# Performance work log

Hardware: AMD Instinct MI355X
Metric: run time of the kernel (lower is better)

The kernel has to match this reference:

```python
import jax, jax.numpy as jnp
import numpy as np

SEQ = 128; HID = 2048; NH = 8; NKV = 2; NREP = NH // NKV; HD = 256; FF = 4096
PLD = 256; NLT = 35; NLAYERS = 8; WIN = 512; FULL_LEN = 2048; PAST = 1024
FULL_LAYERS = {5}  # Gemma3 pattern: full attention when (i+1) % 6 == 0
PLE_PROJ_SCALE = HID ** -0.5
PLE_IN_SCALE = 0.7071067811865476  # rsqrt(2)
NEG = -1e9


def _rms(x, w, eps=1e-6):
    return x * jax.lax.rsqrt(jnp.mean(x * x, -1, keepdims=True) + eps) * w


def _vnorm(x, eps=1e-6):
    return x * jax.lax.rsqrt(jnp.mean(x * x, -1, keepdims=True) + eps)


def _rope(x, cos, sin):
    # x: (1, H, S, hd); cos/sin: (1, S, hd)
    c = cos[:, None]; s = sin[:, None]
    h = x.shape[-1] // 2
    x1, x2 = x[..., :h], x[..., h:]
    return x * c + jnp.concatenate([-x2, x1], -1) * s


def _rope_tables(pos, theta):
    inv = 1.0 / (theta ** (np.arange(0, HD, 2, dtype=np.float32) / HD))
    ang = pos[:, None] * inv[None, :]
    emb = np.concatenate([ang, ang], -1)  # (S, HD)
    return jnp.asarray(np.cos(emb), jnp.float32)[None], jnp.asarray(np.sin(emb), jnp.float32)[None]


def setup_inputs() -> dict:
    key = jax.random.key(0)
    ks = iter(jax.random.split(key, 64))
    f = lambda shape, s=0.02: jax.random.normal(next(ks), shape, dtype=jnp.float32) * s
    inp = {}
    inp['hidden_states'] = f((1, SEQ, HID), 1.0)
    inp['per_layer_raw'] = f((1, SEQ, NLT * PLD), 1.0)
    pos = np.arange(PAST, PAST + SEQ, dtype=np.float32)
    inp['cos_s'], inp['sin_s'] = _rope_tables(pos, 10000.0)
    inp['cos_f'], inp['sin_f'] = _rope_tables(pos, 1000000.0)
    i_s = np.arange(SEQ); j_f = np.arange(FULL_LEN); j_s = np.arange(WIN)
    inp['causal_mask_full'] = jnp.asarray(np.where(j_f[None, :] <= PAST + i_s[:, None], 0.0, NEG).astype(np.float32))[None, None]
    inp['causal_mask_sliding'] = jnp.asarray(np.where(j_s[None, :] <= WIN - SEQ + i_s[:, None], 0.0, NEG).astype(np.float32))[None, None]
    ind = np.zeros((FULL_LEN, SEQ), np.float32); ind[PAST + i_s, i_s] = 1.0
    inp['update_indicator'] = jnp.asarray(ind)[None, None]
    inp['K_sliding'] = f((7, NKV, WIN, HD), 1.0); inp['V_sliding'] = f((7, NKV, WIN, HD), 1.0)
    inp['K_full'] = f((1, NKV, FULL_LEN, HD), 1.0); inp['V_full'] = f((1, NKV, FULL_LEN, HD), 1.0)
    # learned parameters (stacked over the 8 layers)
    inp['Wq'] = f((NLAYERS, HID, NH * HD)); inp['Wk'] = f((NLAYERS, HID, NKV * HD))
    inp['Wv'] = f((NLAYERS, HID, NKV * HD)); inp['Wo'] = f((NLAYERS, NH * HD, HID))
    inp['w_in_ln'] = jnp.ones((NLAYERS, HID)); inp['w_q_norm'] = jnp.ones((NLAYERS, HD))
    inp['w_k_norm'] = jnp.ones((NLAYERS, HD)); inp['w_post_attn_ln'] = jnp.ones((NLAYERS, HID))
    inp['w_pre_ff_ln'] = jnp.ones((NLAYERS, HID))
    inp['Wgate'] = f((NLAYERS, HID, FF)); inp['Wup'] = f((NLAYERS, HID, FF)); inp['Wdown'] = f((NLAYERS, FF, HID))
    inp['w_post_ff_ln'] = jnp.ones((NLAYERS, HID))
    inp['Wple_gate'] = f((NLAYERS, HID, PLD)); inp['Wple_proj'] = f((NLAYERS, PLD, HID))
    inp['w_post_ple_ln'] = jnp.ones((NLAYERS, HID))
    inp['layer_scalar'] = jnp.ones((NLAYERS,))
    inp['Wple_model_proj'] = f((HID, NLT * PLD)); inp['w_ple_norm'] = jnp.ones((PLD,))
    return inp


def _forward(hidden_states, per_layer_raw, cos_s, sin_s, cos_f, sin_f,
             causal_mask_full, causal_mask_sliding, update_indicator,
             K_sliding, V_sliding, K_full, V_full,
             Wq, Wk, Wv, Wo, w_in_ln, w_q_norm, w_k_norm, w_post_attn_ln,
             w_pre_ff_ln, Wgate, Wup, Wdown, w_post_ff_ln,
             Wple_gate, Wple_proj, w_post_ple_ln, layer_scalar,
             Wple_model_proj, w_ple_norm):
    S = hidden_states.shape[1]
    # PLE: project hidden, per-layer RMSNorm over pld groups, combine with raw per-layer inputs
    proj = (hidden_states @ Wple_model_proj) * PLE_PROJ_SCALE  # (1,S,NLT*PLD)
    proj = _rms(proj.reshape(S, NLT, PLD), w_ple_norm)
    raw = per_layer_raw.reshape(S, NLT, PLD)
    ple = ((proj + raw) * PLE_IN_SCALE).reshape(1, S, NLT * PLD)

    hs = hidden_states
    Ks, Vs, Kf, Vf = K_sliding, V_sliding, K_full, V_full
    new_ks, new_vs = [], []
    si = 0; fi = 0
    for i in range(NLAYERS):
        is_full = i in FULL_LAYERS
        cos, sin = (cos_f, sin_f) if is_full else (cos_s, sin_s)
        res = hs
        h = _rms(hs, w_in_ln[i])
        # Q/K norm is per (token, head) RMS over head_dim, then RoPE
        q = _rms((h @ Wq[i]).reshape(1, S, NH, HD), w_q_norm[i]).transpose(0, 2, 1, 3)
        q = _rope(q, cos, sin)
        k = _rms((h @ Wk[i]).reshape(1, S, NKV, HD), w_k_norm[i]).transpose(0, 2, 1, 3)
        k = _rope(k, cos, sin)
        v = _vnorm((h @ Wv[i]).reshape(1, S, NKV, HD).transpose(0, 2, 1, 3))
        new_ks.append(k); new_vs.append(v)
        if is_full:
            # matmul-based indicator scatter into the full-attention cache slot
            k_sc = jnp.matmul(update_indicator, k)  # (1,NKV,FULL_LEN,HD)
            v_sc = jnp.matmul(update_indicator, v)
            cm = jnp.sum(update_indicator, -1, keepdims=True)  # (1,1,FULL_LEN,1)
            Kf = Kf.at[fi:fi + 1].set(Kf[fi:fi + 1] * (1.0 - cm) + k_sc)
            Vf = Vf.at[fi:fi + 1].set(Vf[fi:fi + 1] * (1.0 - cm) + v_sc)
            K_attn, V_attn, mask = Kf[fi:fi + 1], Vf[fi:fi + 1], causal_mask_full
            fi += 1
        else:
            # sliding-window shift: drop oldest S, append new K/V
            nk = jnp.concatenate([Ks[si:si + 1, :, S:, :], k], axis=2)
            nv = jnp.concatenate([Vs[si:si + 1, :, S:, :], v], axis=2)
            Ks = Ks.at[si:si + 1].set(nk); Vs = Vs.at[si:si + 1].set(nv)
            K_attn, V_attn, mask = nk, nv, causal_mask_sliding
            si += 1
        Ke = jnp.repeat(K_attn, NREP, axis=1)  # GQA repeat_interleave
        Ve = jnp.repeat(V_attn, NREP, axis=1)
        aw = jax.nn.softmax(jnp.einsum('bhsd,bhld->bhsl', q, Ke) + mask, axis=-1)  # no 1/sqrt(hd), as in source
        attn = jnp.einsum('bhsl,bhld->bhsd', aw, Ve).transpose(0, 2, 1, 3).reshape(1, S, NH * HD)
        hs = res + _rms(attn @ Wo[i], w_post_attn_ln[i])
        res = hs
        h2 = _rms(hs, w_pre_ff_ln[i])
        mlp = (jax.nn.gelu(h2 @ Wgate[i], approximate=True) * (h2 @ Wup[i])) @ Wdown[i]
        hs = res + _rms(mlp, w_post_ff_ln[i])
        res = hs
        pls = ple[:, :, i * PLD:(i + 1) * PLD]
        g = jax.nn.gelu(hs @ Wple_gate[i], approximate=True) * pls
        hs = res + _rms(g @ Wple_proj[i], w_post_ple_ln[i])
        hs = hs * layer_scalar[i]
    return hs, jnp.stack(new_ks), jnp.stack(new_vs)


def reference(hidden_states, per_layer_raw, cos_s, sin_s, cos_f, sin_f,
              causal_mask_full, causal_mask_sliding, update_indicator,
              K_sliding, V_sliding, K_full, V_full,
              Wq, Wk, Wv, Wo, w_in_ln, w_q_norm, w_k_norm, w_post_attn_ln,
              w_pre_ff_ln, Wgate, Wup, Wdown, w_post_ff_ln,
              Wple_gate, Wple_proj, w_post_ple_ln, layer_scalar,
              Wple_model_proj, w_ple_norm):
    return _forward(hidden_states, per_layer_raw, cos_s, sin_s, cos_f, sin_f,
                    causal_mask_full, causal_mask_sliding, update_indicator,
                    K_sliding, V_sliding, K_full, V_full,
                    Wq, Wk, Wv, Wo, w_in_ln, w_q_norm, w_k_norm, w_post_attn_ln,
                    w_pre_ff_ln, Wgate, Wup, Wdown, w_post_ff_ln,
                    Wple_gate, Wple_proj, w_post_ple_ln, layer_scalar,
                    Wple_model_proj, w_ple_norm)
```

## Files before the change

kernel.cpp:

```cpp
#include <hip/hip_runtime.h>
#include <stdint.h>

typedef short s16x8 __attribute__((ext_vector_type(8)));
typedef float f32x4 __attribute__((ext_vector_type(4)));
typedef unsigned short u16;

#define MFMA16(a,b,c) __builtin_amdgcn_mfma_f32_16x16x32_bf16((a),(b),(c),0,0,0)
#define ACAP 1184

__device__ __forceinline__ u16 f2bf(float f) {
  union { float f; unsigned u; } v; v.f = f;
  return (u16)((v.u + 0x7FFFu + ((v.u >> 16) & 1u)) >> 16);
}
__device__ __forceinline__ float bf2f(u16 u) {
  union { float f; unsigned v; } x; x.v = ((unsigned)u) << 16; return x.f;
}

__device__ __forceinline__ float block_sum256(float v, float* lred) {
  #pragma unroll
  for (int d = 32; d >= 1; d >>= 1) v += __shfl_xor(v, d);
  __syncthreads();
  if ((threadIdx.x & 63) == 0) lred[threadIdx.x >> 6] = v;
  __syncthreads();
  return (lred[0] + lred[1]) + (lred[2] + lred[3]);
}

__device__ __forceinline__ float gelu_t(float x) {
  float u = 0.7978845608028654f * (x + 0.044715f * x * x * x);
  return 0.5f * x * (1.0f + tanhf(u));
}

__global__ __launch_bounds__(256) void gemm3_k(
    const u16* __restrict__ Ah, const u16* __restrict__ Al, int lda,
    const float* __restrict__ W0, const float* __restrict__ W1, const float* __restrict__ W2,
    int e0, int e1, int ld0, int ld1, int ld2,
    float* __restrict__ out, int N, int kchunk, int Ktot)
{
  __shared__ float red[4 * 2048];
  const int n0 = blockIdx.x * 16;
  const int split = blockIdx.y;
  const float* W; int ldw, c0;
  if (n0 < e0)      { W = W0; ldw = ld0; c0 = n0; }
  else if (n0 < e1) { W = W1; ldw = ld1; c0 = n0 - e0; }
  else              { W = W2; ldw = ld2; c0 = n0 - e1; }
  const int w = threadIdx.x >> 6, l = threadIdx.x & 63;
  const int lr = l & 15, lh = l >> 4;
  const int wk = kchunk >> 2;
  const int k0 = split * kchunk + w * wk, k1 = k0 + wk;
  const u16* Abh = Ah + (size_t)lr * lda + 8 * lh;
  const u16* Abl = Al + (size_t)lr * lda + 8 * lh;
  const float* Wb = W + (size_t)(8 * lh) * ldw + (c0 + lr);

  f32x4 acc[8];
  #pragma unroll
  for (int i = 0; i < 8; i++) acc[i] = (f32x4){0.f,0.f,0.f,0.f};

  for (int k = k0; k < k1; k += 32) {
    s16x8 ah[8], al[8];
    #pragma unroll
    for (int mt = 0; mt < 8; mt++) {
      ah[mt] = *(const s16x8*)(Abh + (size_t)(16*mt)*lda + k);
      al[mt] = *(const s16x8*)(Abl + (size_t)(16*mt)*lda + k);
    }
    s16x8 bh, bl;
    #pragma unroll
    for (int jj = 0; jj < 8; jj++) {
      float wv = Wb[(size_t)(k + jj) * ldw];
      u16 hb = f2bf(wv);
      bh[jj] = (short)hb;
      bl[jj] = (short)f2bf(wv - bf2f(hb));
    }
    #pragma unroll
    for (int mt = 0; mt < 8; mt++) acc[mt] = MFMA16(ah[mt], bh, acc[mt]);
    #pragma unroll
    for (int mt = 0; mt < 8; mt++) acc[mt] = MFMA16(ah[mt], bl, acc[mt]);
    #pragma unroll
    for (int mt = 0; mt < 8; mt++) acc[mt] = MFMA16(al[mt], bh, acc[mt]);
  }
  #pragma unroll
  for (int mt = 0; mt < 8; mt++)
    #pragma unroll
    for (int r = 0; r < 4; r++)
      red[w * 2048 + (16*mt + 4*lh + r) * 16 + lr] = acc[mt][r];
  __syncthreads();
  const size_t ob = (size_t)split * (128 * (size_t)N) + n0;
  #pragma unroll
  for (int i = 0; i < 8; i++) {
    int e = threadIdx.x + 256 * i;
    int row = e >> 4, c = e & 15;
    float s = (red[e] + red[2048 + e]) + (red[4096 + e] + red[6144 + e]);
    out[ob + (size_t)row * N + c] = s;
  }
}

__global__ __launch_bounds__(256) void init_k(
    const float* __restrict__ hid, const float* __restrict__ w0,
    float* __restrict__ hs, u16* __restrict__ h0b, u16* __restrict__ h0l,
    u16* __restrict__ hbf, u16* __restrict__ hbl)
{
  __shared__ float lred[4];
  int s = blockIdx.x, t = threadIdx.x;
  float x[8]; float ss = 0.f;
  #pragma unroll
  for (int i = 0; i < 8; i++) {
    int j = t + 256 * i;
    float v = hid[(size_t)s * 2048 + j];
    x[i] = v; ss += v * v;
    hs[(size_t)s * 2048 + j] = v;
    u16 hi = f2bf(v);
    h0b[(size_t)s * 2048 + j] = hi;
    h0l[(size_t)s * 2048 + j] = f2bf(v - bf2f(hi));
  }
  ss = block_sum256(ss, lred);
  float rs = rsqrtf(ss * (1.f/2048.f) + 1e-6f);
  #pragma unroll
  for (int i = 0; i < 8; i++) {
    int j = t + 256 * i;
    float xn = x[i] * rs * w0[j];
    u16 hi = f2bf(xn);
    hbf[(size_t)s * 2048 + j] = hi;
    hbl[(size_t)s * 2048 + j] = f2bf(xn - bf2f(hi));
  }
}

__global__ __launch_bounds__(256) void ple_norm_k(
    const float* __restrict__ proj, const float* __restrict__ raw,
    const float* __restrict__ wp, float* __restrict__ ple)
{
  __shared__ float lred[4];
  int b = blockIdx.x;
  int s = b / 35, lt = b % 35, t = threadIdx.x;
  size_t idx = (size_t)s * 8960 + lt * 256 + t;
  float p = proj[idx] * 0.022097086912079612f;
  float ss = block_sum256(p * p, lred);
  float rs = rsqrtf(ss * (1.f/256.f) + 1e-6f);
  ple[idx] = (p * rs * wp[t] + raw[idx]) * 0.7071067811865476f;
}

__global__ __launch_bounds__(256) void fill_kv2_k(
    const float* __restrict__ oK, const float* __restrict__ oV,
    u16* __restrict__ Kh, u16* __restrict__ Kl,
    u16* __restrict__ VTh, u16* __restrict__ VTl,
    int olen, int ooff, int old_ld, int nA)
{
  __shared__ float tile[64][65];
  int b = blockIdx.x, t = threadIdx.x;
  if (b < nA) {
    size_t base = (size_t)b * 4096;
    #pragma unroll
    for (int i = 0; i < 16; i++) {
      size_t e = base + t + 256 * i;
      int kv = (int)(e / ((size_t)olen * 256));
      size_t rem = e - (size_t)kv * olen * 256;
      int j = (int)(rem >> 8), d = (int)(rem & 255);
      float v = oK[((size_t)kv * old_ld + ooff + j) * 256 + d];
      u16 hi = f2bf(v);
      size_t dst = (size_t)kv * (ACAP*256) + (size_t)j * 256 + d;
      Kh[dst] = hi;
      Kl[dst] = f2bf(v - bf2f(hi));
    }
  } else {
    int tb = b - nA;
    int tj = olen >> 6;
    int per_kv = tj * 4;
    int kv = tb / per_kv, rem = tb % per_kv;
    int j0 = (rem % tj) * 64, d0 = (rem / tj) * 64;
    #pragma unroll
    for (int i = 0; i < 16; i++) {
      int e = t + 256 * i;
      int jj = e >> 6, dd = e & 63;
      tile[jj][dd] = oV[((size_t)kv * old_ld + ooff + j0 + jj) * 256 + d0 + dd];
    }
    __syncthreads();
    #pragma unroll
    for (int i = 0; i < 16; i++) {
      int e = t + 256 * i;
      int dd = e >> 6, jj = e & 63;
      float v = tile[jj][dd];
      u16 hi = f2bf(v);
      size_t dst = (size_t)kv * (256*ACAP) + (size_t)(d0 + dd) * ACAP + (j0 + jj);
      VTh[dst] = hi;
      VTl[dst] = f2bf(v - bf2f(hi));
    }
  }
}

__global__ __launch_bounds__(256) void prep_attn_k(
    const float* __restrict__ qkvP, int nsplit,
    const float* __restrict__ wq, const float* __restrict__ wk,
    const float* __restrict__ cosb, const float* __restrict__ sinb,
    u16* __restrict__ qh, u16* __restrict__ ql,
    float* __restrict__ outk, float* __restrict__ outv,
    u16* __restrict__ Kh, u16* __restrict__ Kl,
    u16* __restrict__ VTh, u16* __restrict__ VTl, int jbase)
{
  __shared__ float lred[4];
  __shared__ float xs[256];
  int s = blockIdx.x, t = threadIdx.x;
  const float* base = qkvP + (size_t)s * 3072;
  float c = cosb[s * 256 + t], sn = sinb[s * 256 + t];
  #pragma unroll 1
  for (int h = 0; h < 8; h++) {
    float v = 0.f;
    for (int sp = 0; sp < nsplit; sp++) v += base[(size_t)sp * (128*3072) + h * 256 + t];
    float ss = block_sum256(v * v, lred);
    float rs = rsqrtf(ss * (1.f/256.f) + 1e-6f);
    float xn = v * rs * wq[t];
    xs[t] = xn;
    __syncthreads();
    float pr = xs[t ^ 128];
    float ro = (t < 128) ? -pr : pr;
    float qv = xn * c + ro * sn;
    u16 hi = f2bf(qv);
    qh[((size_t)h * 128 + s) * 256 + t] = hi;
    ql[((size_t)h * 128 + s) * 256 + t] = f2bf(qv - bf2f(hi));
    __syncthreads();
  }
  #pragma unroll 1
  for (int g = 0; g < 2; g++) {
    float v = 0.f;
    for (int sp = 0; sp < nsplit; sp++) v += base[(size_t)sp * (128*3072) + 2048 + g * 256 + t];
    float ss = block_sum256(v * v, lred);
    float rs = rsqrtf(ss * (1.f/256.f) + 1e-6f);
    float xn = v * rs * wk[t];
    xs[t] = xn;
    __syncthreads();
    float pr = xs[t ^ 128];
    float ro = (t < 128) ? -pr : pr;
    float kq = xn * c + ro * sn;
    outk[(size_t)g * (128*256) + s * 256 + t] = kq;
    u16 khi = f2bf(kq);
    size_t kdst = (size_t)g * (ACAP*256) + (size_t)(jbase + s) * 256 + t;
    Kh[kdst] = khi;
    Kl[kdst] = f2bf(kq - bf2f(khi));
    __syncthreads();
    float vv = 0.f;
    for (int sp = 0; sp < nsplit; sp++) vv += base[(size_t)sp * (128*3072) + 2560 + g * 256 + t];
    float ss2 = block_sum256(vv * vv, lred);
    float rs2 = rsqrtf(ss2 * (1.f/256.f) + 1e-6f);
    float vn = vv * rs2;
    outv[(size_t)g * (128*256) + s * 256 + t] = vn;
    u16 vhi = f2bf(vn);
    size_t vdst = (size_t)g * (256*ACAP) + (size_t)t * ACAP + (jbase + s);
    VTh[vdst] = vhi;
    VTl[vdst] = f2bf(vn - bf2f(vhi));
  }
}

__global__ __launch_bounds__(256, 1) void attn5_k(
    const u16* __restrict__ qh, const u16* __restrict__ ql,
    const u16* __restrict__ Kh, const u16* __restrict__ Kl,
    const u16* __restrict__ VTh, const u16* __restrict__ VTl,
    u16* __restrict__ outbf, u16* __restrict__ outlo, int off)
{
  __shared__ float OW[3][16][256];
  __shared__ float MW[4][16];
  __shared__ float LW[4][16];
  __shared__ u16 Ph[4][16*32];
  __shared__ u16 Pl[4][16*32];
  int bx = blockIdx.x;
  int h = bx >> 3, qt = bx & 7;
  int kv = h >> 2;
  int s0 = qt * 16;
  int nkeys = off + s0 + 16;
  int w = threadIdx.x >> 6, l = threadIdx.x & 63;
  int lr = l & 15, lh = l >> 4;
  int ck = ((nkeys + 127) >> 7) << 5;
  int jb = w * ck;
  int je = min(jb + ck, nkeys);
  const u16* Khb = Kh + (size_t)kv * (ACAP * 256);
  const u16* Klb = Kl + (size_t)kv * (ACAP * 256);
  const u16* Vhb = VTh + (size_t)kv * (256 * (size_t)ACAP);
  const u16* Vlb = VTl + (size_t)kv * (256 * (size_t)ACAP);

  s16x8 aqh[8], aql[8];
  {
    const u16* qrh = qh + ((size_t)h * 128 + s0 + lr) * 256 + 8 * lh;
    const u16* qrl = ql + ((size_t)h * 128 + s0 + lr) * 256 + 8 * lh;
    #pragma unroll
    for (int kk = 0; kk < 8; kk++) {
      aqh[kk] = *(const s16x8*)(qrh + kk * 32);
      aql[kk] = *(const s16x8*)(qrl + kk * 32);
    }
  }
  f32x4 accO[16];
  #pragma unroll
  for (int i = 0; i < 16; i++) accO[i] = (f32x4){0.f,0.f,0.f,0.f};
  float m_run[4], l_run[4];
  #pragma unroll
  for (int r = 0; r < 4; r++) { m_run[r] = -3.0e38f; l_run[r] = 0.f; }
  u16* Pwh = &Ph[w][0];
  u16* Pwl = &Pl[w][0];

  for (int j0 = jb; j0 < je; j0 += 32) {
    f32x4 lg[2];
    lg[0] = (f32x4){0.f,0.f,0.f,0.f};
    lg[1] = (f32x4){0.f,0.f,0.f,0.f};
    #pragma unroll
    for (int kk = 0; kk < 8; kk++) {
      const u16* kb0 = Khb + (size_t)(j0 + lr) * 256 + kk * 32 + 8 * lh;
      const u16* kb1 = Khb + (size_t)(j0 + 16 + lr) * 256 + kk * 32 + 8 * lh;
      const u16* kl0 = Klb + (size_t)(j0 + lr) * 256 + kk * 32 + 8 * lh;
      const u16* kl1 = Klb + (size_t)(j0 + 16 + lr) * 256 + kk * 32 + 8 * lh;
      s16x8 b0h = *(const s16x8*)kb0, b1h = *(const s16x8*)kb1;
      s16x8 b0l = *(const s16x8*)kl0, b1l = *(const s16x8*)kl1;
      lg[0] = MFMA16(aqh[kk], b0h, lg[0]);
      lg[1] = MFMA16(aqh[kk], b1h, lg[1]);
      lg[0] = MFMA16(aqh[kk], b0l, lg[0]);
      lg[1] = MFMA16(aqh[kk], b1l, lg[1]);
      lg[0] = MFMA16(aql[kk], b0h, lg[0]);
      lg[1] = MFMA16(aql[kk], b1h, lg[1]);
    }
    float tmax[4];
    #pragma unroll
    for (int r = 0; r < 4; r++) tmax[r] = -1.0e30f;
    #pragma unroll
    for (int tt = 0; tt < 2; tt++) {
      int j = j0 + 16 * tt + lr;
      #pragma unroll
      for (int r = 0; r < 4; r++)
        if (j <= off + s0 + 4 * lh + r) tmax[r] = fmaxf(tmax[r], lg[tt][r]);
    }
    #pragma unroll
    for (int d = 1; d < 16; d <<= 1)
      #pragma unroll
      for (int r = 0; r < 4; r++) tmax[r] = fmaxf(tmax[r], __shfl_xor(tmax[r], d));
    float scl[4], rsum[4];
    #pragma unroll
    for (int r = 0; r < 4; r++) {
      float mn = fmaxf(m_run[r], tmax[r]);
      scl[r] = __expf(m_run[r] - mn);
      m_run[r] = mn;
      rsum[r] = 0.f;
    }
    #pragma unroll
    for (int tt = 0; tt < 2; tt++) {
      int j = j0 + 16 * tt + lr;
      #pragma unroll
      for (int r = 0; r < 4; r++) {
        bool valid = (j <= off + s0 + 4 * lh + r);
        float p = valid ? __expf(lg[tt][r] - m_run[r]) : 0.f;
        lg[tt][r] = p;
        rsum[r] += p;
      }
    }
    #pragma unroll
    for (int d = 1; d < 16; d <<= 1)
      #pragma unroll
      for (int r = 0; r < 4; r++) rsum[r] += __shfl_xor(rsum[r], d);
    #pragma unroll
    for (int r = 0; r < 4; r++) l_run[r] = l_run[r] * scl[r] + rsum[r];
    #pragma unroll
    for (int tt = 0; tt < 2; tt++) {
      #pragma unroll
      for (int r = 0; r < 4; r++) {
        float p = lg[tt][r];
        u16 phi = f2bf(p);
        Pwh[(4 * lh + r) * 32 + 16 * tt + lr] = phi;
        Pwl[(4 * lh + r) * 32 + 16 * tt + lr] = f2bf(p - bf2f(phi));
      }
    }
    #pragma unroll
    for (int t2 = 0; t2 < 16; t2++)
      #pragma unroll
      for (int r = 0; r < 4; r++) accO[t2][r] *= scl[r];
    s16x8 pah = *(const s16x8*)(Pwh + lr * 32 + 8 * lh);
    s16x8 pal = *(const s16x8*)(Pwl + lr * 32 + 8 * lh);
    #pragma unroll
    for (int t2 = 0; t2 < 16; t2++) {
      s16x8 bvh = *(const s16x8*)(Vhb + (size_t)(16 * t2 + lr) * ACAP + j0 + 8 * lh);
      s16x8 bvl = *(const s16x8*)(Vlb + (size_t)(16 * t2 + lr) * ACAP + j0 + 8 * lh);
      accO[t2] = MFMA16(pah, bvh, accO[t2]);
      accO[t2] = MFMA16(pah, bvl, accO[t2]);
      accO[t2] = MFMA16(pal, bvh, accO[t2]);
    }
  }
  if (w > 0) {
    #pragma unroll
    for (int t2 = 0; t2 < 16; t2++)
      #pragma unroll
      for (int r = 0; r < 4; r++)
        OW[w - 1][4 * lh + r][16 * t2 + lr] = accO[t2][r];
  }
  if (lr == 0) {
    #pragma unroll
    for (int r = 0; r < 4; r++) { MW[w][4 * lh + r] = m_run[r]; LW[w][4 * lh + r] = l_run[r]; }
  }
  __syncthreads();
  if (w == 0) {
    float ew[4][4], inv[4];
    #pragma unroll
    for (int r = 0; r < 4; r++) {
      int row = 4 * lh + r;
      float M = fmaxf(fmaxf(m_run[r], MW[1][row]), fmaxf(MW[2][row], MW[3][row]));
      ew[r][0] = __expf(m_run[r] - M);
      ew[r][1] = __expf(MW[1][row] - M);
      ew[r][2] = __expf(MW[2][row] - M);
      ew[r][3] = __expf(MW[3][row] - M);
      float L = l_run[r] * ew[r][0] + LW[1][row] * ew[r][1] + LW[2][row] * ew[r][2] + LW[3][row] * ew[r][3];
      inv[r] = 1.f / L;
    }
    #pragma unroll
    for (int t2 = 0; t2 < 16; t2++) {
      #pragma unroll
      for (int r = 0; r < 4; r++) {
        int row = 4 * lh + r, c = 16 * t2 + lr;
        float o = accO[t2][r] * ew[r][0] + OW[0][row][c] * ew[r][1]
                + OW[1][row][c] * ew[r][2] + OW[2][row][c] * ew[r][3];
        float val = o * inv[r];
        u16 hi = f2bf(val);
        outbf[(size_t)(s0 + row) * 2048 + h * 256 + c] = hi;
        outlo[(size_t)(s0 + row) * 2048 + h * 256 + c] = f2bf(val - bf2f(hi));
      }
    }
  }
}

__global__ __launch_bounds__(256) void norm_res_k(
    const float* __restrict__ parts, int nsplit,
    const float* __restrict__ wn, float* __restrict__ hs,
    const float* __restrict__ w2, u16* __restrict__ outbf, u16* __restrict__ outlo,
    const float* __restrict__ scp, float* __restrict__ outf)
{
  __shared__ float lred[4];
  int row = blockIdx.x, t = threadIdx.x;
  const float* pr = parts + (size_t)row * 2048;
  float x[8]; float ss = 0.f;
  #pragma unroll
  for (int i = 0; i < 8; i++) {
    int j = t + 256 * i;
    float v = 0.f;
    for (int sp = 0; sp < nsplit; sp++) v += pr[(size_t)sp * (128*2048) + j];
    x[i] = v; ss += v * v;
  }
  ss = block_sum256(ss, lred);
  float rs = rsqrtf(ss * (1.f/2048.f) + 1e-6f);
  float sc = scp ? scp[0] : 1.f;
  float y[8]; float ss2 = 0.f;
  #pragma unroll
  for (int i = 0; i < 8; i++) {
    int j = t + 256 * i;
    float v = (hs[(size_t)row * 2048 + j] + x[i] * rs * wn[j]) * sc;
    y[i] = v; ss2 += v * v;
    hs[(size_t)row * 2048 + j] = v;
    if (outf) outf[(size_t)row * 2048 + j] = v;
  }
  if (outbf) {
    if (w2) {
      ss2 = block_sum256(ss2, lred);
      float rs2 = rsqrtf(ss2 * (1.f/2048.f) + 1e-6f);
      #pragma unroll
      for (int i = 0; i < 8; i++) {
        int j = t + 256 * i;
        float xn = y[i] * rs2 * w2[j];
        u16 hi = f2bf(xn);
        outbf[(size_t)row * 2048 + j] = hi;
        if (outlo) outlo[(size_t)row * 2048 + j] = f2bf(xn - bf2f(hi));
      }
    } else {
      #pragma unroll
      for (int i = 0; i < 8; i++) {
        int j = t + 256 * i;
        u16 hi = f2bf(y[i]);
        outbf[(size_t)row * 2048 + j] = hi;
        if (outlo) outlo[(size_t)row * 2048 + j] = f2bf(y[i] - bf2f(hi));
      }
    }
  }
}

__global__ __launch_bounds__(256) void mlp_act_k(
    const float* __restrict__ gu, int nsplit, u16* __restrict__ out, u16* __restrict__ outlo)
{
  int base = blockIdx.x * 1024 + threadIdx.x * 4;
  int row = base >> 12, j = base & 4095;
  float g[4] = {0,0,0,0}, u[4] = {0,0,0,0};
  for (int sp = 0; sp < nsplit; sp++) {
    const float4 gg = *(const float4*)(gu + (size_t)sp * (128*8192) + (size_t)row * 8192 + j);
    const float4 uu = *(const float4*)(gu + (size_t)sp * (128*8192) + (size_t)row * 8192 + 4096 + j);
    g[0]+=gg.x; g[1]+=gg.y; g[2]+=gg.z; g[3]+=gg.w;
    u[0]+=uu.x; u[1]+=uu.y; u[2]+=uu.z; u[3]+=uu.w;
  }
  size_t ob = (size_t)row * 4096 + j;
  #pragma unroll
  for (int q = 0; q < 4; q++) {
    float val = gelu_t(g[q]) * u[q];
    u16 hi = f2bf(val);
    out[ob + q] = hi;
    outlo[ob + q] = f2bf(val - bf2f(hi));
  }
}

__global__ __launch_bounds__(256) void ple_act_k(
    const float* __restrict__ pgP, int nsplit, const float* __restrict__ ple,
    int layer, u16* __restrict__ gbf, u16* __restrict__ gbl)
{
  int s = blockIdx.x, t = threadIdx.x;
  float x = 0.f;
  for (int sp = 0; sp < nsplit; sp++) x += pgP[(size_t)sp * (128*256) + s * 256 + t];
  float val = gelu_t(x) * ple[(size_t)s * 8960 + layer * 256 + t];
  u16 hi = f2bf(val);
  gbf[s * 256 + t] = hi;
  gbl[s * 256 + t] = f2bf(val - bf2f(hi));
}

extern "C" void kernel_launch(void* const* d_in, const int* in_sizes, int n_in,
                              void* d_out, int out_size, void* d_ws, size_t ws_size,
                              hipStream_t stream)
{
  const float* hid   = (const float*)d_in[0];
  const float* raw   = (const float*)d_in[1];
  const float* cos_s = (const float*)d_in[2];
  const float* sin_s = (const float*)d_in[3];
  const float* cos_f = (const float*)d_in[4];
  const float* sin_f = (const float*)d_in[5];
  const float* Ksl   = (const float*)d_in[9];
  const float* Vsl   = (const float*)d_in[10];
  const float* Kfu   = (const float*)d_in[11];
  const float* Vfu   = (const float*)d_in[12];
  const float* Wq    = (const float*)d_in[13];
  const float* Wk    = (const float*)d_in[14];
  const float* Wv    = (const float*)d_in[15];
  const float* Wo    = (const float*)d_in[16];
  const float* w_in  = (const float*)d_in[17];
  const float* w_qn  = (const float*)d_in[18];
  const float* w_kn  = (const float*)d_in[19];
  const float* w_pa  = (const float*)d_in[20];
  const float* w_pf  = (const float*)d_in[21];
  const float* Wg    = (const float*)d_in[22];
  const float* Wu    = (const float*)d_in[23];
  const float* Wd    = (const float*)d_in[24];
  const float* w_ff  = (const float*)d_in[25];
  const float* Wpg   = (const float*)d_in[26];
  const float* Wpp   = (const float*)d_in[27];
  const float* w_pp  = (const float*)d_in[28];
  const float* lsc   = (const float*)d_in[29];
  const float* Wpm   = (const float*)d_in[30];
  const float* w_pn  = (const float*)d_in[31];

  char* ws = (char*)d_ws;
  size_t off = 0;
  auto alloc = [&](size_t b) { size_t o = off; off += (b + 255) & ~(size_t)255; return o; };
  size_t o_hs   = alloc(128*2048*4);
  size_t o_qkvP = alloc(2ull*128*3072*4);
  size_t o_t1P  = alloc(2ull*128*2048*4);
  size_t o_guP  = alloc(1ull*128*8192*4);
  size_t o_t2P  = alloc(2ull*128*2048*4);
  size_t o_pgP  = alloc(4ull*128*256*4);
  size_t o_t3P  = alloc(1ull*128*2048*4);
  size_t o_ple  = alloc(128ull*8960*4);
  size_t o_h0b  = alloc(128*2048*2);
  size_t o_h0l  = alloc(128*2048*2);
  size_t o_hb   = alloc(128*2048*2);
  size_t o_hbl  = alloc(128*2048*2);
  size_t o_h2b  = alloc(128*2048*2);
  size_t o_h2l  = alloc(128*2048*2);
  size_t o_hrb  = alloc(128*2048*2);
  size_t o_hrl  = alloc(128*2048*2);
  size_t o_ab   = alloc(128*2048*2);
  size_t o_abl  = alloc(128*2048*2);
  size_t o_mb   = alloc(128ull*4096*2);
  size_t o_mbl  = alloc(128ull*4096*2);
  size_t o_gb   = alloc(128*256*2);
  size_t o_gbl  = alloc(128*256*2);
  size_t o_qh   = alloc(8ull*128*256*2);
  size_t o_ql   = alloc(8ull*128*256*2);
  size_t o_Kh   = alloc(2ull*ACAP*256*2);
  size_t o_Kl   = alloc(2ull*ACAP*256*2);
  size_t o_VTh  = alloc(2ull*256*ACAP*2);
  size_t o_VTl  = alloc(2ull*256*ACAP*2);

  float* hs   = (float*)(ws + o_hs);
  float* qkvP = (float*)(ws + o_qkvP);
  float* t1P  = (float*)(ws + o_t1P);
  float* guP  = (float*)(ws + o_guP);
  float* t2P  = (float*)(ws + o_t2P);
  float* pgP  = (float*)(ws + o_pgP);
  float* t3P  = (float*)(ws + o_t3P);
  float* ple  = (float*)(ws + o_ple);
  float* proj = (float*)(ws + o_qkvP);
  u16* h0b = (u16*)(ws + o_h0b);
  u16* h0l = (u16*)(ws + o_h0l);
  u16* hb  = (u16*)(ws + o_hb);
  u16* hbl = (u16*)(ws + o_hbl);
  u16* h2b = (u16*)(ws + o_h2b);
  u16* h2l = (u16*)(ws + o_h2l);
  u16* hrb = (u16*)(ws + o_hrb);
  u16* hrl = (u16*)(ws + o_hrl);
  u16* ab  = (u16*)(ws + o_ab);
  u16* abl = (u16*)(ws + o_abl);
  u16* mb  = (u16*)(ws + o_mb);
  u16* mbl = (u16*)(ws + o_mbl);
  u16* gb  = (u16*)(ws + o_gb);
  u16* gbl = (u16*)(ws + o_gbl);
  u16* qhb = (u16*)(ws + o_qh);
  u16* qlb = (u16*)(ws + o_ql);
  u16* Khc = (u16*)(ws + o_Kh);
  u16* Klc = (u16*)(ws + o_Kl);
  u16* VThc = (u16*)(ws + o_VTh);
  u16* VTlc = (u16*)(ws + o_VTl);

  float* ouths = (float*)d_out;
  float* outk  = ouths + 128*2048;
  float* outv  = outk + 8*2*128*256;

  init_k<<<128, 256, 0, stream>>>(hid, w_in, hs, h0b, h0l, hb, hbl);
  gemm3_k<<<dim3(560,1), 256, 0, stream>>>(h0b, h0l, 2048, Wpm, Wpm, Wpm,
      8960, 8960, 8960, 8960, 8960, proj, 8960, 2048, 2048);
  ple_norm_k<<<128*35, 256, 0, stream>>>(proj, raw, w_pn, ple);

  for (int i = 0; i < 8; i++) {
    bool full = (i == 5);
    int si = (i < 5) ? i : i - 1;
    const float* cs = full ? cos_f : cos_s;
    const float* sn = full ? sin_f : sin_s;
    int jbase = full ? 1024 : 384;
    if (full) {
      fill_kv2_k<<<256, 256, 0, stream>>>(Kfu, Vfu, Khc, Klc, VThc, VTlc, 1024, 0, 2048, 128);
    } else {
      fill_kv2_k<<<96, 256, 0, stream>>>(Ksl + (size_t)si*2*512*256, Vsl + (size_t)si*2*512*256,
                                         Khc, Klc, VThc, VTlc, 384, 128, 512, 48);
    }
    gemm3_k<<<dim3(192,2), 256, 0, stream>>>(hb, hbl, 2048,
        Wq + (size_t)i*2048*2048, Wk + (size_t)i*2048*512, Wv + (size_t)i*2048*512,
        2048, 2560, 2048, 512, 512, qkvP, 3072, 1024, 2048);
    prep_attn_k<<<128, 256, 0, stream>>>(qkvP, 2, w_qn + i*256, w_kn + i*256, cs, sn,
        qhb, qlb, outk + (size_t)i*65536, outv + (size_t)i*65536, Khc, Klc, VThc, VTlc, jbase);
    attn5_k<<<64, 256, 0, stream>>>(qhb, qlb, Khc, Klc, VThc, VTlc, ab, abl, jbase);
    gemm3_k<<<dim3(128,2), 256, 0, stream>>>(ab, abl, 2048,
        Wo + (size_t)i*2048*2048, Wo, Wo, 2048, 2048, 2048, 2048, 2048,
        t1P, 2048, 1024, 2048);
    norm_res_k<<<128, 256, 0, stream>>>(t1P, 2, w_pa + i*2048, hs,
        w_pf + i*2048, h2b, h2l, nullptr, nullptr);
    gemm3_k<<<dim3(512,1), 256, 0, stream>>>(h2b, h2l, 2048,
        Wg + (size_t)i*2048*4096, Wu + (size_t)i*2048*4096, Wu,
        4096, 8192, 4096, 4096, 4096, guP, 8192, 2048, 2048);
    mlp_act_k<<<512, 256, 0, stream>>>(guP, 1, mb, mbl);
    gemm3_k<<<dim3(128,2), 256, 0, stream>>>(mb, mbl, 4096,
        Wd + (size_t)i*4096*2048, Wd, Wd, 2048, 2048, 2048, 2048, 2048,
        t2P, 2048, 2048, 4096);
    norm_res_k<<<128, 256, 0, stream>>>(t2P, 2, w_ff + i*2048, hs,
        nullptr, hrb, hrl, nullptr, nullptr);
    gemm3_k<<<dim3(16,4), 256, 0, stream>>>(hrb, hrl, 2048,
        Wpg + (size_t)i*2048*256, Wpg, Wpg, 256, 256, 256, 256, 256,
        pgP, 256, 512, 2048);
    ple_act_k<<<128, 256, 0, stream>>>(pgP, 4, ple, i, gb, gbl);
    gemm3_k<<<dim3(128,1), 256, 0, stream>>>(gb, gbl, 256,
        Wpp + (size_t)i*256*2048, Wpp, Wpp, 2048, 2048, 2048, 2048, 2048,
        t3P, 2048, 256, 256);
    norm_res_k<<<128, 256, 0, stream>>>(t3P, 1, w_pp + i*2048, hs,
        (i < 7) ? (w_in + (i+1)*2048) : nullptr,
        (i < 7) ? hb : nullptr,
        (i < 7) ? hbl : nullptr,
        lsc + i, (i == 7) ? ouths : nullptr);
  }
}
```

Measured before the change: 2.604 ms.

## Split attention keys across four blocks with combine kernel; prefetch GEMM weights

Attention now launches 256 blocks instead of 64, each covering a quarter of the key range. Partial unnormalized outputs plus max and sum statistics go to a workspace, and a new combine kernel merges them into the bf16 hi/lo output. This targets low occupancy, since 64 blocks on a many-CU GPU leave most units idle, at the cost of an extra launch and fp32 partial traffic. Separately, the split-bf16 GEMM now software-prefetches the next K-step's weight values into registers to hide global load latency.

```diff
diff --git a/kernel.cpp b/kernel.cpp
--- a/kernel.cpp
+++ b/kernel.cpp
@@ -55,6 +55,10 @@
   #pragma unroll
   for (int i = 0; i < 8; i++) acc[i] = (f32x4){0.f,0.f,0.f,0.f};
 
+  float bc[8];
+  #pragma unroll
+  for (int jj = 0; jj < 8; jj++) bc[jj] = Wb[(size_t)(k0 + jj) * ldw];
+
   for (int k = k0; k < k1; k += 32) {
     s16x8 ah[8], al[8];
     #pragma unroll
@@ -62,13 +66,17 @@
       ah[mt] = *(const s16x8*)(Abh + (size_t)(16*mt)*lda + k);
       al[mt] = *(const s16x8*)(Abl + (size_t)(16*mt)*lda + k);
     }
+    float bn[8];
+    if (k + 32 < k1) {
+      #pragma unroll
+      for (int jj = 0; jj < 8; jj++) bn[jj] = Wb[(size_t)(k + 32 + jj) * ldw];
+    }
     s16x8 bh, bl;
     #pragma unroll
     for (int jj = 0; jj < 8; jj++) {
-      float wv = Wb[(size_t)(k + jj) * ldw];
-      u16 hb = f2bf(wv);
+      u16 hb = f2bf(bc[jj]);
       bh[jj] = (short)hb;
-      bl[jj] = (short)f2bf(wv - bf2f(hb));
+      bl[jj] = (short)f2bf(bc[jj] - bf2f(hb));
     }
     #pragma unroll
     for (int mt = 0; mt < 8; mt++) acc[mt] = MFMA16(ah[mt], bh, acc[mt]);
@@ -76,6 +84,10 @@
     for (int mt = 0; mt < 8; mt++) acc[mt] = MFMA16(ah[mt], bl, acc[mt]);
     #pragma unroll
     for (int mt = 0; mt < 8; mt++) acc[mt] = MFMA16(al[mt], bh, acc[mt]);
+    if (k + 32 < k1) {
+      #pragma unroll
+      for (int jj = 0; jj < 8; jj++) bc[jj] = bn[jj];
+    }
   }
   #pragma unroll
   for (int mt = 0; mt < 8; mt++)
@@ -247,11 +259,11 @@
   }
 }
 
-__global__ __launch_bounds__(256, 1) void attn5_k(
+__global__ __launch_bounds__(256) void attn6_k(
     const u16* __restrict__ qh, const u16* __restrict__ ql,
     const u16* __restrict__ Kh, const u16* __restrict__ Kl,
     const u16* __restrict__ VTh, const u16* __restrict__ VTl,
-    u16* __restrict__ outbf, u16* __restrict__ outlo, int off)
+    float* __restrict__ Opart, float* __restrict__ ML, int off)
 {
   __shared__ float OW[3][16][256];
   __shared__ float MW[4][16];
@@ -259,15 +271,18 @@
   __shared__ u16 Ph[4][16*32];
   __shared__ u16 Pl[4][16*32];
   int bx = blockIdx.x;
-  int h = bx >> 3, qt = bx & 7;
+  int ks = bx & 3;
+  int b64 = bx >> 2;
+  int h = b64 >> 3, qt = b64 & 7;
   int kv = h >> 2;
   int s0 = qt * 16;
   int nkeys = off + s0 + 16;
   int w = threadIdx.x >> 6, l = threadIdx.x & 63;
   int lr = l & 15, lh = l >> 4;
-  int ck = ((nkeys + 127) >> 7) << 5;
-  int jb = w * ck;
-  int je = min(jb + ck, nkeys);
+  int cw = ((nkeys + 511) >> 9) << 5;
+  int g = ks * 4 + w;
+  int jb = g * cw;
+  int je = min(jb + cw, nkeys);
   const u16* Khb = Kh + (size_t)kv * (ACAP * 256);
   const u16* Klb = Kl + (size_t)kv * (ACAP * 256);
   const u16* Vhb = VTh + (size_t)kv * (256 * (size_t)ACAP);
@@ -388,7 +403,8 @@
   }
   __syncthreads();
   if (w == 0) {
-    float ew[4][4], inv[4];
+    float ew[4][4];
+    float Mrow[4], Lrow[4];
     #pragma unroll
     for (int r = 0; r < 4; r++) {
       int row = 4 * lh + r;
@@ -397,9 +413,10 @@
       ew[r][1] = __expf(MW[1][row] - M);
       ew[r][2] = __expf(MW[2][row] - M);
       ew[r][3] = __expf(MW[3][row] - M);
-      float L = l_run[r] * ew[r][0] + LW[1][row] * ew[r][1] + LW[2][row] * ew[r][2] + LW[3][row] * ew[r][3];
-      inv[r] = 1.f / L;
-    }
+      Lrow[r] = l_run[r] * ew[r][0] + LW[1][row] * ew[r][1] + LW[2][row] * ew[r][2] + LW[3][row] * ew[r][3];
+      Mrow[r] = M;
+    }
+    float* Ob = Opart + (size_t)bx * 4096;
     #pragma unroll
     for (int t2 = 0; t2 < 16; t2++) {
       #pragma unroll
@@ -407,12 +424,47 @@
         int row = 4 * lh + r, c = 16 * t2 + lr;
         float o = accO[t2][r] * ew[r][0] + OW[0][row][c] * ew[r][1]
                 + OW[1][row][c] * ew[r][2] + OW[2][row][c] * ew[r][3];
-        float val = o * inv[r];
-        u16 hi = f2bf(val);
-        outbf[(size_t)(s0 + row) * 2048 + h * 256 + c] = hi;
-        outlo[(size_t)(s0 + row) * 2048 + h * 256 + c] = f2bf(val - bf2f(hi));
+        Ob[row * 256 + c] = o;
       }
     }
+    if (lr == 0) {
+      #pragma unroll
+      for (int r = 0; r < 4; r++) {
+        int row = 4 * lh + r;
+        ML[bx * 32 + row] = Mrow[r];
+        ML[bx * 32 + 16 + row] = Lrow[r];
+      }
+    }
+  }
+}
+
+__global__ __launch_bounds__(256) void attn_comb_k(
+    const float* __restrict__ Opart, const float* __restrict__ ML,
+    u16* __restrict__ outbf, u16* __restrict__ outlo)
+{
+  int b = blockIdx.x;
+  int h = b >> 3, qt = b & 7, s0 = qt * 16;
+  int c = threadIdx.x;
+  #pragma unroll 1
+  for (int row = 0; row < 16; row++) {
+    float m[4], lv[4];
+    #pragma unroll
+    for (int ks = 0; ks < 4; ks++) {
+      m[ks]  = ML[(b * 4 + ks) * 32 + row];
+      lv[ks] = ML[(b * 4 + ks) * 32 + 16 + row];
+    }
+    float Mg = fmaxf(fmaxf(m[0], m[1]), fmaxf(m[2], m[3]));
+    float L = 0.f, o = 0.f;
+    #pragma unroll
+    for (int ks = 0; ks < 4; ks++) {
+      float e = __expf(m[ks] - Mg);
+      L += lv[ks] * e;
+      o += Opart[((size_t)(b * 4 + ks)) * 4096 + row * 256 + c] * e;
+    }
+    float val = o / L;
+    u16 hi = f2bf(val);
+    outbf[(size_t)(s0 + row) * 2048 + h * 256 + c] = hi;
+    outlo[(size_t)(s0 + row) * 2048 + h * 256 + c] = f2bf(val - bf2f(hi));
   }
 }
 
@@ -569,6 +621,8 @@
   size_t o_Kl   = alloc(2ull*ACAP*256*2);
   size_t o_VTh  = alloc(2ull*256*ACAP*2);
   size_t o_VTl  = alloc(2ull*256*ACAP*2);
+  size_t o_Op   = alloc(256ull*4096*4);
+  size_t o_ML   = alloc(256ull*32*4);
 
   float* hs   = (float*)(ws + o_hs);
   float* qkvP = (float*)(ws + o_qkvP);
@@ -599,6 +653,8 @@
   u16* Klc = (u16*)(ws + o_Kl);
   u16* VThc = (u16*)(ws + o_VTh);
   u16* VTlc = (u16*)(ws + o_VTl);
+  float* Opart = (float*)(ws + o_Op);
+  float* MLb   = (float*)(ws + o_ML);
 
   float* ouths = (float*)d_out;
   float* outk  = ouths + 128*2048;
@@ -626,7 +682,8 @@
         2048, 2560, 2048, 512, 512, qkvP, 3072, 1024, 2048);
     prep_attn_k<<<128, 256, 0, stream>>>(qkvP, 2, w_qn + i*256, w_kn + i*256, cs, sn,
         qhb, qlb, outk + (size_t)i*65536, outv + (size_t)i*65536, Khc, Klc, VThc, VTlc, jbase);
-    attn5_k<<<64, 256, 0, stream>>>(qhb, qlb, Khc, Klc, VThc, VTlc, ab, abl, jbase);
+    attn6_k<<<256, 256, 0, stream>>>(qhb, qlb, Khc, Klc, VThc, VTlc, Opart, MLb, jbase);
+    attn_comb_k<<<64, 256, 0, stream>>>(Opart, MLb, ab, abl);
     gemm3_k<<<dim3(128,2), 256, 0, stream>>>(ab, abl, 2048,
         Wo + (size_t)i*2048*2048, Wo, Wo, 2048, 2048, 2048, 2048, 2048,
         t1P, 2048, 1024, 2048);
```

Result: faster. 2.324 ms (-10.7%).
